# Performance work log

Hardware: AMD Instinct MI355X
Metric: run time of the kernel (lower is better)

## Reference

```python
import jax, jax.numpy as jnp
import numpy as np

N_NODES = 50000
N_EDGES = 1600000
IN_DIM, HID, HEADS, OUT_DIM = 128, 32, 4, 16
NEG_SLOPE = 0.2  # DGL GATConv default


def setup_inputs() -> dict:
    key = jax.random.key(0)
    ks = jax.random.split(key, 12)
    features = jax.random.normal(ks[0], (N_NODES, IN_DIM), dtype=jnp.float32)
    src = jax.random.randint(ks[1], (N_EDGES,), 0, N_NODES, dtype=jnp.int32)
    dst = jax.random.randint(ks[2], (N_EDGES,), 0, N_NODES, dtype=jnp.int32)
    # layer 1 params (xavier-style scale)
    W1 = jax.random.normal(ks[3], (IN_DIM, HEADS * HID), dtype=jnp.float32) * (2.0 / (IN_DIM + HEADS * HID)) ** 0.5
    al1 = jax.random.normal(ks[4], (HEADS, HID), dtype=jnp.float32) * 0.1
    ar1 = jax.random.normal(ks[5], (HEADS, HID), dtype=jnp.float32) * 0.1
    b1 = jnp.zeros((HEADS * HID,), dtype=jnp.float32)
    # layer 2 params
    W2 = jax.random.normal(ks[6], (HID, OUT_DIM), dtype=jnp.float32) * (2.0 / (HID + OUT_DIM)) ** 0.5
    al2 = jax.random.normal(ks[7], (1, OUT_DIM), dtype=jnp.float32) * 0.1
    ar2 = jax.random.normal(ks[8], (1, OUT_DIM), dtype=jnp.float32) * 0.1
    b2 = jnp.zeros((OUT_DIM,), dtype=jnp.float32)
    return {"features": features, "src": src, "dst": dst,
            "W1": W1, "al1": al1, "ar1": ar1, "b1": b1,
            "W2": W2, "al2": al2, "ar2": ar2, "b2": b2}


def gat_conv(x, src, dst, W, al, ar, b, n_nodes):
    """DGL GATConv (no dropout, no residual). Returns [N, H, out]."""
    H, out = al.shape
    feat = (x @ W).reshape(-1, H, out)                       # [N,H,out]
    el = jnp.sum(feat * al, axis=-1)                         # [N,H]
    er = jnp.sum(feat * ar, axis=-1)                         # [N,H]
    e = jax.nn.leaky_relu(el[src] + er[dst], NEG_SLOPE)      # [E,H]
    # segment softmax over incoming edges per destination node
    m = jax.ops.segment_max(e, dst, num_segments=n_nodes)    # [N,H]
    ex = jnp.exp(e - m[dst])                                 # [E,H]
    s = jax.ops.segment_sum(ex, dst, num_segments=n_nodes)   # [N,H]
    alpha = ex / s[dst]                                      # [E,H]
    msg = alpha[:, :, None] * feat[src]                      # [E,H,out]
    rst = jax.ops.segment_sum(msg, dst, num_segments=n_nodes)
    return rst + b.reshape(H, out)


def reference(features, src, dst, W1, al1, ar1, b1, W2, al2, ar2, b2):
    n = features.shape[0]
    x1 = gat_conv(features, src, dst, W1, al1, ar1, b1, n)   # [N,HEADS,HID]
    x1 = jnp.mean(jax.nn.relu(x1), axis=1)                   # [N,HID]
    x2 = gat_conv(x1, src, dst, W2, al2, ar2, b2, n)         # [N,1,OUT]
    x2 = jnp.squeeze(x2, axis=1)                             # [N,OUT]
    return jax.nn.log_softmax(x2, axis=-1)
```

## Files before the change

### kernel.cpp

```cpp
#include <hip/hip_runtime.h>
#include <math.h>

#define NEG_SLOPE 0.2f
#define BINCAP 10240

typedef __attribute__((ext_vector_type(8))) short short8;
typedef __attribute__((ext_vector_type(4))) float f32x4;
typedef __attribute__((ext_vector_type(2))) float f32x2;

__device__ __forceinline__ float lrelu(float x) {
    return x >= 0.f ? x : NEG_SLOPE * x;
}
__device__ __forceinline__ unsigned bf16_rne(float f) {
    unsigned b = __float_as_uint(f);
    return (b + 0x7FFFu + ((b >> 16) & 1u)) >> 16;
}

extern "C" __global__ __launch_bounds__(256) void gemm_scatter(
    const float* __restrict__ X, const float* __restrict__ W1,
    const float* __restrict__ al, const float* __restrict__ ar,
    const int* __restrict__ src, const int* __restrict__ dst,
    int* __restrict__ bin_cursor, unsigned* __restrict__ binned,
    unsigned short* __restrict__ feat1b, float* __restrict__ el1,
    float* __restrict__ er1, int N, int E, int nbins, int gemm_blocks)
{
    extern __shared__ char smem_raw[];
    int tid = threadIdx.x;

    if ((int)blockIdx.x >= gemm_blocks) {
        unsigned* stage = (unsigned*)smem_raw;
        int* hist   = (int*)(stage + 3328);
        int* base_l = hist + 256;
        int bid = blockIdx.x - gemm_blocks;
        hist[tid] = 0;
        __syncthreads();
        int epb = (E + 511) / 512;
        int beg = bid * epb, end = min(E, beg + epb);
        int cnt_local = end - beg;
        for (int k = tid; k < cnt_local; k += 256) {
            int d = dst[beg + k];
            stage[k] = ((unsigned)d << 16) | (unsigned)src[beg + k];
            atomicAdd(&hist[d >> 8], 1);
        }
        __syncthreads();
        if (tid < nbins) {
            int c = hist[tid];
            base_l[tid] = (c > 0) ? (tid * BINCAP + atomicAdd(&bin_cursor[tid], c)) : 0;
        }
        __syncthreads();
        hist[tid] = 0;
        __syncthreads();
        for (int k = tid; k < cnt_local; k += 256) {
            unsigned w = stage[k];
            int bin = w >> 24;
            int slot = atomicAdd(&hist[bin], 1);
            binned[base_l[bin] + slot] = w;
        }
        return;
    }

    unsigned short* Xb = (unsigned short*)smem_raw;
    unsigned short* Wb = Xb + 64 * 136;
    int nb = blockIdx.x * 64;

    for (int idx = tid; idx < 128 * 128; idx += 256) {
        int kin = idx >> 7, nout = idx & 127;
        Wb[nout * 138 + kin] = (unsigned short)bf16_rne(W1[idx]);
    }
    for (int idx = tid; idx < 64 * 32; idx += 256) {
        int row = idx >> 5, q = idx & 31;
        int n = nb + row;
        float4 v = (n < N) ? *(const float4*)&X[(size_t)n * 128 + q * 4]
                           : make_float4(0.f, 0.f, 0.f, 0.f);
        unsigned lo = bf16_rne(v.x) | (bf16_rne(v.y) << 16);
        unsigned hi = bf16_rne(v.z) | (bf16_rne(v.w) << 16);
        *(uint2*)&Xb[row * 136 + q * 4] = make_uint2(lo, hi);
    }
    __syncthreads();

    int wave = tid >> 6, lane = tid & 63;
    int m = lane & 15, quad = lane >> 4;
    f32x4 acc[8];
#pragma unroll
    for (int t = 0; t < 8; ++t) acc[t] = (f32x4){0.f, 0.f, 0.f, 0.f};

#pragma unroll
    for (int kt = 0; kt < 4; ++kt) {
        int k0 = kt * 32 + quad * 8;
        short8 a = *(const short8*)&Xb[(wave * 16 + m) * 136 + k0];
#pragma unroll
        for (int t = 0; t < 8; ++t) {
            short8 b = *(const short8*)&Wb[(t * 16 + m) * 138 + k0];
            acc[t] = __builtin_amdgcn_mfma_f32_16x16x32_bf16(a, b, acc[t], 0, 0, 0);
        }
    }

    float al_lo[4], al_hi[4], ar_lo[4], ar_hi[4];
#pragma unroll
    for (int h = 0; h < 4; ++h) {
        al_lo[h] = al[h * 32 + m];       al_hi[h] = al[h * 32 + 16 + m];
        ar_lo[h] = ar[h * 32 + m];       ar_hi[h] = ar[h * 32 + 16 + m];
    }

#pragma unroll
    for (int r = 0; r < 4; ++r) {
        int n = nb + wave * 16 + quad * 4 + r;
        float pel[4], per[4];
#pragma unroll
        for (int h = 0; h < 4; ++h) {
            float fa = acc[2 * h][r], fb = acc[2 * h + 1][r];
            pel[h] = fa * al_lo[h] + fb * al_hi[h];
            per[h] = fa * ar_lo[h] + fb * ar_hi[h];
        }
#pragma unroll
        for (int off = 1; off < 16; off <<= 1) {
#pragma unroll
            for (int h = 0; h < 4; ++h) {
                pel[h] += __shfl_xor(pel[h], off);
                per[h] += __shfl_xor(per[h], off);
            }
        }
        if (n < N) {
#pragma unroll
            for (int t = 0; t < 8; ++t)
                feat1b[(size_t)n * 128 + t * 16 + m] =
                    (unsigned short)bf16_rne(acc[t][r]);
            if (m == 0) {
#pragma unroll
                for (int h = 0; h < 4; ++h) {
                    el1[(size_t)n * 4 + h] = pel[h];
                    er1[(size_t)n * 4 + h] = per[h];
                }
            }
        }
    }
}

__global__ __launch_bounds__(256) void local_sort(
    const unsigned* __restrict__ binned, const int* __restrict__ bin_cursor,
    int* __restrict__ rowptr, unsigned short* __restrict__ deg,
    unsigned short* __restrict__ csr, int N, int nbins)
{
    __shared__ int cnt[256];
    __shared__ int sh[256];
    int b = blockIdx.x;
    int t = threadIdx.x;
    int gbase = b * BINCAP;
    int gcount = bin_cursor[b];
    cnt[t] = 0;
    __syncthreads();
    for (int i = t; i < gcount; i += 256)
        atomicAdd(&cnt[(binned[gbase + i] >> 16) & 255], 1);
    __syncthreads();
    int own = cnt[t];
    sh[t] = own;
    __syncthreads();
#pragma unroll
    for (int off = 1; off < 256; off <<= 1) {
        int v = (t >= off) ? sh[t - off] : 0;
        __syncthreads();
        sh[t] += v;
        __syncthreads();
    }
    int excl = sh[t] - own;
    int dcount = min(256, N - (b << 8));
    if (t < dcount) {
        rowptr[(b << 8) + t] = gbase + excl;
        deg[(b << 8) + t] = (unsigned short)own;
    }
    cnt[t] = excl;
    __syncthreads();
    for (int i = t; i < gcount; i += 256) {
        unsigned w = binned[gbase + i];
        int slot = atomicAdd(&cnt[(w >> 16) & 255], 1);
        csr[gbase + slot] = (unsigned short)(w & 0xFFFFu);
    }
}

__global__ __launch_bounds__(256) void agg1_fused(
    const int* __restrict__ rowptr, const unsigned short* __restrict__ deg,
    const unsigned short* __restrict__ csr,
    const unsigned short* __restrict__ feat1b, const float* __restrict__ el1,
    const float* __restrict__ er1, const float* __restrict__ b1,
    const float* __restrict__ W2, const float* __restrict__ al2,
    const float* __restrict__ ar2, unsigned short* __restrict__ feat2b,
    float* __restrict__ el2, float* __restrict__ er2, int N)
{
    __shared__ uint2 pairs[4][4][66];
    int gid = blockIdx.x * 256 + threadIdx.x;
    int d = gid >> 6;
    if (d >= N) return;
    int wv = (threadIdx.x >> 6) & 3;
    int lane = threadIdx.x & 63;
    int h = lane >> 4;
    float4 er4 = ((const float4*)er1)[d];
    int beg = rowptr[d], end = beg + (int)deg[d];
    const unsigned* feat32 = (const unsigned*)feat1b;

    float M = -INFINITY, S = 0.f;
    f32x2 A = {0.f, 0.f};

    for (int base = beg; base < end; base += 64) {
        int cnt = min(64, end - base);
        int sn = 0;
        float4 v = make_float4(-INFINITY, -INFINITY, -INFINITY, -INFINITY);
        if (lane < cnt) {
            sn = (int)csr[base + lane];
            float4 el4 = ((const float4*)el1)[sn];
            v.x = lrelu(el4.x + er4.x);
            v.y = lrelu(el4.y + er4.y);
            v.z = lrelu(el4.z + er4.z);
            v.w = lrelu(el4.w + er4.w);
        }
        float4 cm = v;
#pragma unroll
        for (int off = 1; off < 64; off <<= 1) {
            cm.x = fmaxf(cm.x, __shfl_xor(cm.x, off));
            cm.y = fmaxf(cm.y, __shfl_xor(cm.y, off));
            cm.z = fmaxf(cm.z, __shfl_xor(cm.z, off));
            cm.w = fmaxf(cm.w, __shfl_xor(cm.w, off));
        }
        float4 w;
        w.x = __expf(v.x - cm.x);
        w.y = __expf(v.y - cm.y);
        w.z = __expf(v.z - cm.z);
        w.w = __expf(v.w - cm.w);
        unsigned snb = (unsigned)sn << 6;
        pairs[wv][0][lane] = make_uint2(snb, __float_as_uint(w.x));
        pairs[wv][1][lane] = make_uint2(snb, __float_as_uint(w.y));
        pairs[wv][2][lane] = make_uint2(snb, __float_as_uint(w.z));
        pairs[wv][3][lane] = make_uint2(snb, __float_as_uint(w.w));

        float cmh = (h & 2) ? ((h & 1) ? cm.w : cm.z) : ((h & 1) ? cm.y : cm.x);
        float nM = fmaxf(M, cmh);
        float so = __expf(M - nM);
        float sc = __expf(cmh - nM);
        M = nM;

        f32x2 ca = {0.f, 0.f}, cb = {0.f, 0.f};
        float cs0 = 0.f, cs1 = 0.f;
        int i = 0;
        for (; i + 4 <= cnt; i += 4) {
            uint2 p0 = pairs[wv][h][i];
            uint2 p1 = pairs[wv][h][i + 1];
            uint2 p2 = pairs[wv][h][i + 2];
            uint2 p3 = pairs[wv][h][i + 3];
            unsigned u0 = feat32[p0.x + lane];
            unsigned u1 = feat32[p1.x + lane];
            unsigned u2 = feat32[p2.x + lane];
            unsigned u3 = feat32[p3.x + lane];
            float w0 = __uint_as_float(p0.y), w1 = __uint_as_float(p1.y);
            float w2 = __uint_as_float(p2.y), w3 = __uint_as_float(p3.y);
            ca += (f32x2){w0, w0} * (f32x2){__uint_as_float(u0 << 16),
                                            __uint_as_float(u0 & 0xFFFF0000u)};
            cb += (f32x2){w1, w1} * (f32x2){__uint_as_float(u1 << 16),
                                            __uint_as_float(u1 & 0xFFFF0000u)};
            ca += (f32x2){w2, w2} * (f32x2){__uint_as_float(u2 << 16),
                                            __uint_as_float(u2 & 0xFFFF0000u)};
            cb += (f32x2){w3, w3} * (f32x2){__uint_as_float(u3 << 16),
                                            __uint_as_float(u3 & 0xFFFF0000u)};
            cs0 += w0 + w2;
            cs1 += w1 + w3;
        }
        for (; i < cnt; ++i) {
            uint2 p = pairs[wv][h][i];
            float wb = __uint_as_float(p.y);
            unsigned u = feat32[p.x + lane];
            ca += (f32x2){wb, wb} * (f32x2){__uint_as_float(u << 16),
                                            __uint_as_float(u & 0xFFFF0000u)};
            cs0 += wb;
        }
        ca += cb;
        float cs = cs0 + cs1;
        S = S * so + cs * sc;
        A = A * (f32x2){so, so} + ca * (f32x2){sc, sc};
    }
    float inv = (end > beg) ? (1.f / S) : 0.f;
    float o0 = A.x * inv, o1 = A.y * inv;

    int dim0 = lane * 2;
    float2 bb = *(const float2*)(b1 + dim0);
    float r0 = fmaxf(o0 + bb.x, 0.f);
    float r1 = fmaxf(o1 + bb.y, 0.f);
    r0 += __shfl_xor(r0, 16); r0 += __shfl_xor(r0, 32);
    r1 += __shfl_xor(r1, 16); r1 += __shfl_xor(r1, 32);
    float u0 = 0.25f * r0;
    float u1 = 0.25f * r1;

    int j = lane & 15;
    float f2 = 0.f;
#pragma unroll
    for (int i2 = 0; i2 < 16; ++i2) {
        float xa = __shfl(u0, i2);
        float xb = __shfl(u1, i2);
        f2 += xa * W2[(2 * i2) * 16 + j] + xb * W2[(2 * i2 + 1) * 16 + j];
    }
    float pel = f2 * al2[j], per = f2 * ar2[j];
#pragma unroll
    for (int off = 1; off < 16; off <<= 1) {
        pel += __shfl_xor(pel, off);
        per += __shfl_xor(per, off);
    }
    if (lane < 16) feat2b[(size_t)d * 16 + j] = (unsigned short)bf16_rne(f2);
    if (lane == 0) { el2[d] = pel; er2[d] = per; }
}

__global__ __launch_bounds__(256) void agg2_fused(
    const int* __restrict__ rowptr, const unsigned short* __restrict__ deg,
    const unsigned short* __restrict__ csr,
    const unsigned short* __restrict__ feat2b, const float* __restrict__ el2,
    const float* __restrict__ er2, const float* __restrict__ b2,
    float* __restrict__ out, int N)
{
    __shared__ uint2 pairs2[4][64];
    int gid = blockIdx.x * 256 + threadIdx.x;
    int d = gid >> 6;
    if (d >= N) return;
    int wv = (threadIdx.x >> 6) & 3;
    int lane = threadIdx.x & 63;
    int sub = lane >> 4, dim = lane & 15;
    float er = er2[d];
    int beg = rowptr[d], end = beg + (int)deg[d];

    float M = -INFINITY, S = 0.f, a = 0.f;
    for (int cb = beg; cb < end; cb += 64) {
        int cnt = min(64, end - cb);
        int sn = 0;
        float v = -INFINITY;
        if (lane < cnt) {
            sn = (int)csr[cb + lane];
            v = lrelu(el2[sn] + er);
        }
        float cm = v;
#pragma unroll
        for (int off = 1; off < 64; off <<= 1)
            cm = fmaxf(cm, __shfl_xor(cm, off));
        float w = __expf(v - cm);
        float cs = w;
#pragma unroll
        for (int off = 1; off < 64; off <<= 1)
            cs += __shfl_xor(cs, off);
        pairs2[wv][lane] = make_uint2((unsigned)sn << 4, __float_as_uint(w));

        float nM = fmaxf(M, cm);
        float so = __expf(M - nM);
        float sc = __expf(cm - nM);
        M = nM;
        float ca = 0.f, ca2 = 0.f;
        int i = sub;
        for (; i + 4 < cnt; i += 8) {
            uint2 p0 = pairs2[wv][i];
            uint2 p1 = pairs2[wv][i + 4];
            unsigned u0 = (unsigned)feat2b[p0.x + dim];
            unsigned u1 = (unsigned)feat2b[p1.x + dim];
            ca  += __uint_as_float(p0.y) * __uint_as_float(u0 << 16);
            ca2 += __uint_as_float(p1.y) * __uint_as_float(u1 << 16);
        }
        if (i < cnt) {
            uint2 p = pairs2[wv][i];
            unsigned u = (unsigned)feat2b[p.x + dim];
            ca += __uint_as_float(p.y) * __uint_as_float(u << 16);
        }
        S = S * so + cs * sc;
        a = a * so + (ca + ca2) * sc;
    }
    a += __shfl_xor(a, 16);
    a += __shfl_xor(a, 32);
    float inv = (end > beg) ? (1.f / S) : 0.f;
    float val = a * inv + b2[dim];
    float mm = val;
#pragma unroll
    for (int off = 1; off < 16; off <<= 1)
        mm = fmaxf(mm, __shfl_xor(mm, off));
    float ex = __expf(val - mm);
    float ssum = ex;
#pragma unroll
    for (int off = 1; off < 16; off <<= 1)
        ssum += __shfl_xor(ssum, off);
    if (lane < 16)
        out[(size_t)d * 16 + dim] = val - (mm + __logf(ssum));
}

extern "C" void kernel_launch(void* const* d_in, const int* in_sizes, int n_in,
                              void* d_out, int out_size, void* d_ws, size_t ws_size,
                              hipStream_t stream)
{
    const float* X   = (const float*)d_in[0];
    const int*   src = (const int*)d_in[1];
    const int*   dst = (const int*)d_in[2];
    const float* W1  = (const float*)d_in[3];
    const float* al1 = (const float*)d_in[4];
    const float* ar1 = (const float*)d_in[5];
    const float* b1  = (const float*)d_in[6];
    const float* W2  = (const float*)d_in[7];
    const float* al2 = (const float*)d_in[8];
    const float* ar2 = (const float*)d_in[9];
    const float* b2  = (const float*)d_in[10];
    int N = in_sizes[0] / 128;
    int E = in_sizes[1];
    int nbins = (N + 255) >> 8;

    float* ws = (float*)d_ws;
    size_t o = 0;
    unsigned short* feat1b = (unsigned short*)(ws + o); o += (size_t)N * 64;
    float* el1   = ws + o; o += (size_t)N * 4;
    float* er1   = ws + o; o += (size_t)N * 4;
    unsigned short* feat2b = (unsigned short*)(ws + o); o += (size_t)N * 8;
    float* el2   = ws + o; o += (size_t)N;
    float* er2   = ws + o; o += (size_t)N;
    int* rowptr  = (int*)(ws + o); o += (size_t)N;
    unsigned short* deg = (unsigned short*)(ws + o); o += (size_t)N / 2 + 1;
    int* bin_cursor = (int*)(ws + o); o += 256;
    unsigned* binned = (unsigned*)(ws + o); o += (size_t)nbins * BINCAP;
    unsigned short* csr = (unsigned short*)(ws + o); o += (size_t)nbins * BINCAP / 2 + 1;
    float* out = (float*)d_out;

    hipMemsetAsync(bin_cursor, 0, 256 * sizeof(int), stream);

    int gemm_blocks = (N + 63) / 64;
    gemm_scatter<<<gemm_blocks + 512, 256, 52736, stream>>>(
        X, W1, al1, ar1, src, dst, bin_cursor, binned,
        feat1b, el1, er1, N, E, nbins, gemm_blocks);

    local_sort<<<nbins, 256, 0, stream>>>(binned, bin_cursor, rowptr, deg, csr, N, nbins);

    agg1_fused<<<(N * 64 + 255) / 256, 256, 0, stream>>>(
        rowptr, deg, csr, feat1b, el1, er1, b1, W2, al2, ar2, feat2b, el2, er2, N);

    agg2_fused<<<(N * 64 + 255) / 256, 256, 0, stream>>>(
        rowptr, deg, csr, feat2b, el2, er2, b2, out, N);
}
```

Baseline: 248.0 us.

## Amortize W1 staging over four tiles, widen local sort, split layer-2 matvec

The GEMM blocks now handle four 64-row tiles each, so the bf16 conversion and transposition of W1 into shared memory runs once per 256 nodes instead of once per 64. The local sort kernel uses 512 threads and replaces its barrier-heavy 256-step shared-memory scan with a wave-shuffle scan plus per-wave sums. In agg1, the 32x16 W2 matvec is split across the four lane groups, each doing 4 of the 16 iterations, then combined with xor shuffles. The trade-off is fewer GEMM blocks, and so less parallelism, in exchange for fewer redundant W1 loads.

```diff
diff --git a/kernel.cpp b/kernel.cpp
--- a/kernel.cpp
+++ b/kernel.cpp
@@ -61,39 +61,14 @@
 
     unsigned short* Xb = (unsigned short*)smem_raw;
     unsigned short* Wb = Xb + 64 * 136;
-    int nb = blockIdx.x * 64;
 
     for (int idx = tid; idx < 128 * 128; idx += 256) {
         int kin = idx >> 7, nout = idx & 127;
         Wb[nout * 138 + kin] = (unsigned short)bf16_rne(W1[idx]);
     }
-    for (int idx = tid; idx < 64 * 32; idx += 256) {
-        int row = idx >> 5, q = idx & 31;
-        int n = nb + row;
-        float4 v = (n < N) ? *(const float4*)&X[(size_t)n * 128 + q * 4]
-                           : make_float4(0.f, 0.f, 0.f, 0.f);
-        unsigned lo = bf16_rne(v.x) | (bf16_rne(v.y) << 16);
-        unsigned hi = bf16_rne(v.z) | (bf16_rne(v.w) << 16);
-        *(uint2*)&Xb[row * 136 + q * 4] = make_uint2(lo, hi);
-    }
-    __syncthreads();
 
     int wave = tid >> 6, lane = tid & 63;
     int m = lane & 15, quad = lane >> 4;
-    f32x4 acc[8];
-#pragma unroll
-    for (int t = 0; t < 8; ++t) acc[t] = (f32x4){0.f, 0.f, 0.f, 0.f};
-
-#pragma unroll
-    for (int kt = 0; kt < 4; ++kt) {
-        int k0 = kt * 32 + quad * 8;
-        short8 a = *(const short8*)&Xb[(wave * 16 + m) * 136 + k0];
-#pragma unroll
-        for (int t = 0; t < 8; ++t) {
-            short8 b = *(const short8*)&Wb[(t * 16 + m) * 138 + k0];
-            acc[t] = __builtin_amdgcn_mfma_f32_16x16x32_bf16(a, b, acc[t], 0, 0, 0);
-        }
-    }
 
     float al_lo[4], al_hi[4], ar_lo[4], ar_hi[4];
 #pragma unroll
@@ -102,75 +77,109 @@
         ar_lo[h] = ar[h * 32 + m];       ar_hi[h] = ar[h * 32 + 16 + m];
     }
 
-#pragma unroll
-    for (int r = 0; r < 4; ++r) {
-        int n = nb + wave * 16 + quad * 4 + r;
-        float pel[4], per[4];
-#pragma unroll
-        for (int h = 0; h < 4; ++h) {
-            float fa = acc[2 * h][r], fb = acc[2 * h + 1][r];
-            pel[h] = fa * al_lo[h] + fb * al_hi[h];
-            per[h] = fa * ar_lo[h] + fb * ar_hi[h];
-        }
-#pragma unroll
-        for (int off = 1; off < 16; off <<= 1) {
+    for (int t4 = 0; t4 < 4; ++t4) {
+        int nb = blockIdx.x * 256 + t4 * 64;
+        if (nb >= N) break;
+        __syncthreads();
+        for (int idx = tid; idx < 64 * 32; idx += 256) {
+            int row = idx >> 5, q = idx & 31;
+            int n = nb + row;
+            float4 v = (n < N) ? *(const float4*)&X[(size_t)n * 128 + q * 4]
+                               : make_float4(0.f, 0.f, 0.f, 0.f);
+            unsigned lo = bf16_rne(v.x) | (bf16_rne(v.y) << 16);
+            unsigned hi = bf16_rne(v.z) | (bf16_rne(v.w) << 16);
+            *(uint2*)&Xb[row * 136 + q * 4] = make_uint2(lo, hi);
+        }
+        __syncthreads();
+
+        f32x4 acc[8];
+#pragma unroll
+        for (int t = 0; t < 8; ++t) acc[t] = (f32x4){0.f, 0.f, 0.f, 0.f};
+
+#pragma unroll
+        for (int kt = 0; kt < 4; ++kt) {
+            int k0 = kt * 32 + quad * 8;
+            short8 a = *(const short8*)&Xb[(wave * 16 + m) * 136 + k0];
+#pragma unroll
+            for (int t = 0; t < 8; ++t) {
+                short8 b = *(const short8*)&Wb[(t * 16 + m) * 138 + k0];
+                acc[t] = __builtin_amdgcn_mfma_f32_16x16x32_bf16(a, b, acc[t], 0, 0, 0);
+            }
+        }
+
+#pragma unroll
+        for (int r = 0; r < 4; ++r) {
+            int n = nb + wave * 16 + quad * 4 + r;
+            float pel[4], per[4];
 #pragma unroll
             for (int h = 0; h < 4; ++h) {
-                pel[h] += __shfl_xor(pel[h], off);
-                per[h] += __shfl_xor(per[h], off);
+                float fa = acc[2 * h][r], fb = acc[2 * h + 1][r];
+                pel[h] = fa * al_lo[h] + fb * al_hi[h];
+                per[h] = fa * ar_lo[h] + fb * ar_hi[h];
             }
-        }
-        if (n < N) {
-#pragma unroll
-            for (int t = 0; t < 8; ++t)
-                feat1b[(size_t)n * 128 + t * 16 + m] =
-                    (unsigned short)bf16_rne(acc[t][r]);
-            if (m == 0) {
+#pragma unroll
+            for (int off = 1; off < 16; off <<= 1) {
 #pragma unroll
                 for (int h = 0; h < 4; ++h) {
-                    el1[(size_t)n * 4 + h] = pel[h];
-                    er1[(size_t)n * 4 + h] = per[h];
+                    pel[h] += __shfl_xor(pel[h], off);
+                    per[h] += __shfl_xor(per[h], off);
                 }
             }
-        }
-    }
-}
-
-__global__ __launch_bounds__(256) void local_sort(
+            if (n < N) {
+#pragma unroll
+                for (int t = 0; t < 8; ++t)
+                    feat1b[(size_t)n * 128 + t * 16 + m] =
+                        (unsigned short)bf16_rne(acc[t][r]);
+                if (m == 0) {
+#pragma unroll
+                    for (int h = 0; h < 4; ++h) {
+                        el1[(size_t)n * 4 + h] = pel[h];
+                        er1[(size_t)n * 4 + h] = per[h];
+                    }
+                }
+            }
+        }
+    }
+}
+
+__global__ __launch_bounds__(512) void local_sort(
     const unsigned* __restrict__ binned, const int* __restrict__ bin_cursor,
     int* __restrict__ rowptr, unsigned short* __restrict__ deg,
     unsigned short* __restrict__ csr, int N, int nbins)
 {
     __shared__ int cnt[256];
-    __shared__ int sh[256];
+    __shared__ int wsum[4];
     int b = blockIdx.x;
     int t = threadIdx.x;
     int gbase = b * BINCAP;
     int gcount = bin_cursor[b];
-    cnt[t] = 0;
+    if (t < 256) cnt[t] = 0;
     __syncthreads();
-    for (int i = t; i < gcount; i += 256)
+    for (int i = t; i < gcount; i += 512)
         atomicAdd(&cnt[(binned[gbase + i] >> 16) & 255], 1);
     __syncthreads();
-    int own = cnt[t];
-    sh[t] = own;
+    int own = (t < 256) ? cnt[t] : 0;
+    int x = own;
+#pragma unroll
+    for (int off = 1; off < 64; off <<= 1) {
+        int y = __shfl_up(x, off);
+        if ((t & 63) >= off) x += y;
+    }
+    if (t < 256 && (t & 63) == 63) wsum[t >> 6] = x;
     __syncthreads();
-#pragma unroll
-    for (int off = 1; off < 256; off <<= 1) {
-        int v = (t >= off) ? sh[t - off] : 0;
-        __syncthreads();
-        sh[t] += v;
-        __syncthreads();
-    }
-    int excl = sh[t] - own;
-    int dcount = min(256, N - (b << 8));
-    if (t < dcount) {
-        rowptr[(b << 8) + t] = gbase + excl;
-        deg[(b << 8) + t] = (unsigned short)own;
-    }
-    cnt[t] = excl;
+    if (t < 256) {
+        int wadd = 0;
+        for (int wv = 0; wv < (t >> 6); ++wv) wadd += wsum[wv];
+        int excl = x + wadd - own;
+        int dcount = min(256, N - (b << 8));
+        if (t < dcount) {
+            rowptr[(b << 8) + t] = gbase + excl;
+            deg[(b << 8) + t] = (unsigned short)own;
+        }
+        cnt[t] = excl;
+    }
     __syncthreads();
-    for (int i = t; i < gcount; i += 256) {
+    for (int i = t; i < gcount; i += 512) {
         unsigned w = binned[gbase + i];
         int slot = atomicAdd(&cnt[(w >> 16) & 255], 1);
         csr[gbase + slot] = (unsigned short)(w & 0xFFFFu);
@@ -290,11 +299,15 @@
     int j = lane & 15;
     float f2 = 0.f;
 #pragma unroll
-    for (int i2 = 0; i2 < 16; ++i2) {
+    for (int t = 0; t < 4; ++t) {
+        int i2 = h * 4 + t;
         float xa = __shfl(u0, i2);
         float xb = __shfl(u1, i2);
         f2 += xa * W2[(2 * i2) * 16 + j] + xb * W2[(2 * i2 + 1) * 16 + j];
     }
+    f2 += __shfl_xor(f2, 16);
+    f2 += __shfl_xor(f2, 32);
+
     float pel = f2 * al2[j], per = f2 * ar2[j];
 #pragma unroll
     for (int off = 1; off < 16; off <<= 1) {
@@ -417,12 +430,12 @@
 
     hipMemsetAsync(bin_cursor, 0, 256 * sizeof(int), stream);
 
-    int gemm_blocks = (N + 63) / 64;
+    int gemm_blocks = (N + 255) / 256;
     gemm_scatter<<<gemm_blocks + 512, 256, 52736, stream>>>(
         X, W1, al1, ar1, src, dst, bin_cursor, binned,
         feat1b, el1, er1, N, E, nbins, gemm_blocks);
 
-    local_sort<<<nbins, 256, 0, stream>>>(binned, bin_cursor, rowptr, deg, csr, N, nbins);
+    local_sort<<<nbins, 512, 0, stream>>>(binned, bin_cursor, rowptr, deg, csr, N, nbins);
 
     agg1_fused<<<(N * 64 + 255) / 256, 256, 0, stream>>>(
         rowptr, deg, csr, feat1b, el1, er1, b1, W2, al2, ar2, feat2b, el2, er2, N);
```

New measurement: 260.1 us. 1.05x slower.
